# Kernel tuning notes

Hardware: AMD Instinct MI355X
Metric: run time of the kernel (lower is better)

Reference implementation:

```python
import jax, jax.numpy as jnp
import numpy as np

B, T, D, H, Dh, ROT = 2, 2048, 2048, 16, 128, 64
DFF = 4 * D
EPS = 1e-5
NEG = -1e9


def setup_inputs() -> dict:
    key = jax.random.key(0)
    ks = jax.random.split(key, 8)
    s = lambda k, shape, sc: jax.random.normal(k, shape, jnp.float32) * sc
    return {
        "x": s(ks[0], (B, T, D), 1.0),
        "ln_scale": jnp.ones((D,), jnp.float32),
        "ln_offset": jnp.zeros((D,), jnp.float32),
        "wq": s(ks[1], (D, D), 0.02),
        "wk": s(ks[2], (D, D), 0.02),
        "wv": s(ks[3], (D, D), 0.02),
        "wo": s(ks[4], (D, D), 0.02),
        "w1": s(ks[5], (D, DFF), 0.02),
        "b1": jnp.zeros((DFF,), jnp.float32),
        "w2": s(ks[6], (DFF, D), 0.02),
        "b2": jnp.zeros((D,), jnp.float32),
    }


def reference(x, ln_scale, ln_offset, wq, wk, wv, wo, w1, b1, w2, b2):
    def ln(h):  # ReplicatedLayerNorm, fp32 internal; note: same params used twice (shared self.norm)
        h32 = h.astype(jnp.float32)
        m = jnp.mean(h32, axis=-1, keepdims=True)
        v = jnp.var(h32, axis=-1, keepdims=True)
        y = (h32 - m) * jax.lax.rsqrt(v + EPS)
        return (y * ln_scale + ln_offset).astype(h.dtype)

    xn = ln(x)
    q = (xn @ wq).reshape(B, T, H, Dh)
    k = (xn @ wk).reshape(B, T, H, Dh)
    v = (xn @ wv).reshape(B, T, H, Dh)

    # GPT-J interleaved RoPE on first ROT dims
    pos = jnp.arange(T, dtype=jnp.float32)
    inv_freq = 1.0 / (10000.0 ** (jnp.arange(0, ROT, 2, dtype=jnp.float32) / ROT))
    freqs = pos[:, None] * inv_freq[None, :]            # (T, ROT/2)
    cos = jnp.repeat(jnp.cos(freqs), 2, axis=-1)[None, :, None, :]  # (1,T,1,ROT)
    sin = jnp.repeat(jnp.sin(freqs), 2, axis=-1)[None, :, None, :]

    def rope(t):
        tr, tp = t[..., :ROT], t[..., ROT:]
        x1 = tr[..., 0::2]
        x2 = tr[..., 1::2]
        rot_half = jnp.stack((-x2, x1), axis=-1).reshape(tr.shape)
        return jnp.concatenate([tr * cos + rot_half * sin, tp], axis=-1)

    q, k = rope(q), rope(k)

    scale = 1.0 / jnp.sqrt(jnp.float32(Dh))
    scores = jnp.einsum('bthd,bshd->bhts', q, k) * scale
    mask = jnp.where(jnp.tril(jnp.ones((T, T), bool)), 0.0, NEG).astype(scores.dtype)
    w = jax.nn.softmax(scores + mask, axis=-1)
    ctx = jnp.einsum('bhts,bshd->bthd', w, v).reshape(B, T, D)
    x1_ = x + ctx @ wo

    xn2 = ln(x1_)
    h = jax.nn.gelu(xn2.astype(jnp.float32) @ w1 + b1)  # default approximate gelu, as in source
    ff = (h @ w2 + b2).astype(x.dtype)
    return x1_ + ff
```

## Files before the change

kernel.cpp:

```cpp
#include <hip/hip_runtime.h>
#include <hip/hip_bf16.h>

#define B_   2
#define T_   2048
#define D_   2048
#define H_   16
#define DH_  128
#define DFF_ 8192

typedef __attribute__((ext_vector_type(8))) short bf16x8;
typedef __attribute__((ext_vector_type(4))) float f32x4;

__device__ __forceinline__ short f2bf(float f) {
    __hip_bfloat16 h = __float2bfloat16(f);
    return *reinterpret_cast<short*>(&h);
}

__device__ __forceinline__ void gload_lds16(const void* g, void* l) {
    __builtin_amdgcn_global_load_lds(
        (const __attribute__((address_space(1))) void*)g,
        (__attribute__((address_space(3))) void*)l,
        16, 0, 0);
}

__device__ __forceinline__ float gelu_tanh(float x) {
    float x3 = x * x * x;
    return 0.5f * x * (1.f + tanhf(0.7978845608028654f * (x + 0.044715f * x3)));
}

#define MFMA32(a, b, c) __builtin_amdgcn_mfma_f32_16x16x32_bf16((a), (b), (c), 0, 0, 0)

__global__ __launch_bounds__(256) void transpose_cvt(const float* __restrict__ in,
                                                     __hip_bfloat16* __restrict__ out,
                                                     int K, int N, int out_ld, int out_row0)
{
    __shared__ float t[32][65];
    const int n0 = blockIdx.x * 64, k0 = blockIdx.y * 32;
    const int tid = threadIdx.x;
    {
        int kr = tid >> 4;
        int nc = (tid & 15) * 4;
        const float* src = in + (size_t)(k0 + kr) * N + n0 + nc;
        float4 a = *reinterpret_cast<const float4*>(src);
        float4 b = *reinterpret_cast<const float4*>(src + (size_t)16 * N);
        t[kr][nc] = a.x; t[kr][nc + 1] = a.y; t[kr][nc + 2] = a.z; t[kr][nc + 3] = a.w;
        t[kr + 16][nc] = b.x; t[kr + 16][nc + 1] = b.y; t[kr + 16][nc + 2] = b.z; t[kr + 16][nc + 3] = b.w;
    }
    __syncthreads();
    {
        int n  = tid >> 2;
        int kc = (tid & 3) * 8;
        __hip_bfloat16 ob[8];
#pragma unroll
        for (int j = 0; j < 8; ++j) ob[j] = __float2bfloat16(t[kc + j][n]);
        *reinterpret_cast<uint4*>(out + (size_t)(out_row0 + n0 + n) * out_ld + k0 + kc) =
            *reinterpret_cast<uint4*>(ob);
    }
}

__global__ __launch_bounds__(256) void ln_kernel(const float* __restrict__ x,
                                                 const float* __restrict__ sc,
                                                 const float* __restrict__ of,
                                                 __hip_bfloat16* __restrict__ out)
{
    int row = blockIdx.x, tid = threadIdx.x;
    const float* xr = x + (size_t)row * D_;
    float4 v0 = reinterpret_cast<const float4*>(xr)[tid * 2];
    float4 v1 = reinterpret_cast<const float4*>(xr)[tid * 2 + 1];
    float vv[8] = {v0.x, v0.y, v0.z, v0.w, v1.x, v1.y, v1.z, v1.w};
    float s = 0.f, ss = 0.f;
#pragma unroll
    for (int j = 0; j < 8; ++j) { s += vv[j]; ss += vv[j] * vv[j]; }
    for (int o = 32; o; o >>= 1) { s += __shfl_down(s, o); ss += __shfl_down(ss, o); }
    __shared__ float red[8];
    int wid = tid >> 6, lane = tid & 63;
    if (!lane) { red[wid] = s; red[4 + wid] = ss; }
    __syncthreads();
    s  = red[0] + red[1] + red[2] + red[3];
    ss = red[4] + red[5] + red[6] + red[7];
    float mean = s * (1.f / D_);
    float var  = ss * (1.f / D_) - mean * mean;
    float rstd = rsqrtf(var + 1e-5f);
    int c0 = tid * 8;
    __hip_bfloat16 ob[8];
#pragma unroll
    for (int j = 0; j < 8; ++j)
        ob[j] = __float2bfloat16((vv[j] - mean) * rstd * sc[c0 + j] + of[c0 + j]);
    *reinterpret_cast<uint4*>(out + (size_t)row * D_ + c0) = *reinterpret_cast<uint4*>(ob);
}

template<int EPI, int BM>
__global__ __launch_bounds__(512, 2) void gemm8p(
    const __hip_bfloat16* __restrict__ A, const __hip_bfloat16* __restrict__ BT,
    void* __restrict__ Cout, const float* __restrict__ bias,
    const float* __restrict__ resid, int M, int N, int K)
{
    constexpr int MFR = BM / 32;
    constexpr int AUL = BM / 128;
    constexpr int VMC = AUL + 2;
    __shared__ short As[2 * 2 * BM * 32];
    __shared__ short Bs[2 * 2 * 256 * 32];

    const int tid = threadIdx.x;
    const int wid = tid >> 6, lane = tid & 63;
    const int lo = lane & 15, hi = lane >> 4;
    const int wr = wid >> 2, wc = wid & 3;

    const int gx = gridDim.x;
    const int nwg = gx * gridDim.y;
    const int bid = blockIdx.y * gx + blockIdx.x;
    const int swz = (bid & 7) * (nwg >> 3) + (bid >> 3);
    const int m0 = (swz / gx) * BM, n0 = (swz % gx) * 256;

    auto stageA = [&](int tt, int ks) {
#pragma unroll
        for (int l = 0; l < AUL; ++l) {
            int c    = l * 512 + tid;
            int row  = c >> 2, ksub = c & 3;
            int kc   = tt * 64 + ks * 32 + ((ksub ^ ((row >> 1) & 3)) << 3);
            int c0   = l * 512 + wid * 64;
            gload_lds16(A + (size_t)(m0 + row) * K + kc,
                        (char*)As + ((tt & 1) * 2 + ks) * (BM * 64) + c0 * 16);
        }
    };
    auto stageB = [&](int tt, int ks) {
#pragma unroll
        for (int l = 0; l < 2; ++l) {
            int c    = l * 512 + tid;
            int row  = c >> 2, ksub = c & 3;
            int kc   = tt * 64 + ks * 32 + ((ksub ^ ((row >> 1) & 3)) << 3);
            int c0   = l * 512 + wid * 64;
            gload_lds16(BT + (size_t)(n0 + row) * K + kc,
                        (char*)Bs + ((tt & 1) * 2 + ks) * 16384 + c0 * 16);
        }
    };

    const int fsw  = (hi ^ ((lo >> 1) & 3)) << 4;
    const int arow = wr * (BM / 2) + lo;
    const int brow = wc * 64 + lo;

    f32x4 acc[MFR][4] = {};
    const int NT = K >> 6;

    stageA(0, 0); stageB(0, 0); stageA(0, 1); stageB(0, 1);
    asm volatile("s_waitcnt vmcnt(%0)" :: "i"(VMC) : "memory");
    __builtin_amdgcn_s_barrier();
    __builtin_amdgcn_sched_barrier(0);

#define PHASE_MFMA(J)                                                         \
        __builtin_amdgcn_s_barrier();                                         \
        asm volatile("s_waitcnt lgkmcnt(0)" ::: "memory");                    \
        __builtin_amdgcn_sched_barrier(0);                                    \
        __builtin_amdgcn_s_setprio(1);                                        \
        _Pragma("unroll")                                                     \
        for (int m = 0; m < MFR; ++m) {                                       \
            acc[m][J]     = MFMA32(af[m], b0, acc[m][J]);                     \
            acc[m][J + 1] = MFMA32(af[m], b1, acc[m][J + 1]);                 \
        }                                                                     \
        __builtin_amdgcn_s_setprio(0);

#pragma unroll 2
    for (int t = 0; t < NT; ++t) {
        const int bsel = t & 1;
        const bool pf = (t + 1 < NT);
        const char* Ab = (const char*)As + bsel * (2 * BM * 64);
        const char* Bb = (const char*)Bs + bsel * 32768;
        bf16x8 af[MFR], b0, b1;

#pragma unroll
        for (int m = 0; m < MFR; ++m)
            af[m] = *reinterpret_cast<const bf16x8*>(Ab + (arow + m * 16) * 64 + fsw);
        b0 = *reinterpret_cast<const bf16x8*>(Bb + brow * 64 + fsw);
        b1 = *reinterpret_cast<const bf16x8*>(Bb + (brow + 16) * 64 + fsw);
        if (pf) stageA(t + 1, 0);
        PHASE_MFMA(0)
        __builtin_amdgcn_s_barrier();
        __builtin_amdgcn_sched_barrier(0);

        b0 = *reinterpret_cast<const bf16x8*>(Bb + (brow + 32) * 64 + fsw);
        b1 = *reinterpret_cast<const bf16x8*>(Bb + (brow + 48) * 64 + fsw);
        if (pf) stageB(t + 1, 0);
        PHASE_MFMA(2)
        asm volatile("s_waitcnt vmcnt(%0)" :: "i"(VMC) : "memory");
        __builtin_amdgcn_s_barrier();
        __builtin_amdgcn_sched_barrier(0);

#pragma unroll
        for (int m = 0; m < MFR; ++m)
            af[m] = *reinterpret_cast<const bf16x8*>(Ab + BM * 64 + (arow + m * 16) * 64 + fsw);
        b0 = *reinterpret_cast<const bf16x8*>(Bb + 16384 + brow * 64 + fsw);
        b1 = *reinterpret_cast<const bf16x8*>(Bb + 16384 + (brow + 16) * 64 + fsw);
        if (pf) stageA(t + 1, 1);
        PHASE_MFMA(0)
        __builtin_amdgcn_s_barrier();
        __builtin_amdgcn_sched_barrier(0);

        b0 = *reinterpret_cast<const bf16x8*>(Bb + 16384 + (brow + 32) * 64 + fsw);
        b1 = *reinterpret_cast<const bf16x8*>(Bb + 16384 + (brow + 48) * 64 + fsw);
        if (pf) stageB(t + 1, 1);
        PHASE_MFMA(2)
        asm volatile("s_waitcnt vmcnt(%0)" :: "i"(VMC) : "memory");
        __builtin_amdgcn_s_barrier();
        __builtin_amdgcn_sched_barrier(0);
    }
#undef PHASE_MFMA

    float* Cf = (float*)Cout;
    __hip_bfloat16* Cb = (__hip_bfloat16*)Cout;
#pragma unroll
    for (int m = 0; m < MFR; ++m) {
        int rbase = m0 + wr * (BM / 2) + m * 16 + hi * 4;
#pragma unroll
        for (int j = 0; j < 4; ++j) {
            int col = n0 + wc * 64 + (j >> 1) * 32 + (j & 1) * 16 + lo;
            float bv = (EPI == 2 || EPI == 3) ? bias[col] : 0.f;
#pragma unroll
            for (int i = 0; i < 4; ++i) {
                size_t idx = (size_t)(rbase + i) * N + col;
                float v = acc[m][j][i];
                if (EPI == 2 || EPI == 3) v += bv;
                if (EPI == 2) v = gelu_tanh(v);
                if (EPI == 1 || EPI == 3) v += resid[idx];
                if (EPI == 0 || EPI == 2) Cb[idx] = __float2bfloat16(v);
                else                      Cf[idx] = v;
            }
        }
    }
}

__global__ __launch_bounds__(256) void rope_kernel(__hip_bfloat16* __restrict__ qkv)
{
    int idx = blockIdx.x * 256 + threadIdx.x;
    int p  = idx & 31;
    int h  = (idx >> 5) & (H_ - 1);
    int bt = idx >> 9;
    int t  = bt & (T_ - 1);
    float invf = exp2f((float)p * -0.4152410118609203f);
    float fr = (float)t * invf;
    float cs, sn;
    __sincosf(fr, &sn, &cs);
    size_t base = (size_t)bt * (3 * D_) + h * DH_ + 2 * p;
#pragma unroll
    for (int qk = 0; qk < 2; ++qk) {
        uint* pp = reinterpret_cast<uint*>(qkv + base + qk * D_);
        uint u = *pp;
        float x1 = __uint_as_float(u << 16);
        float x2 = __uint_as_float(u & 0xffff0000u);
        short r0 = f2bf(x1 * cs - x2 * sn);
        short r1 = f2bf(x2 * cs + x1 * sn);
        *pp = ((uint)(unsigned short)r0) | (((uint)(unsigned short)r1) << 16);
    }
}

__global__ __launch_bounds__(512) void attn_kernel(const __hip_bfloat16* __restrict__ qkv,
                                                   __hip_bfloat16* __restrict__ ctx)
{
    constexpr int LDQ = 3 * D_;
    constexpr int SV  = 68;

    int idx = blockIdx.y * 16 + blockIdx.x;
    int swz = (idx & 7) * 64 + (idx >> 3);
    const int bh  = swz >> 4;
    const int bxr = 15 - (swz & 15);
    const int b = bh >> 4, h = bh & 15;
    const int tq0 = bxr * 128;

    const int tid = threadIdx.x, wid = tid >> 6, lane = tid & 63;
    const int lo = lane & 15, hi = lane >> 4;
    const int t0 = tq0 + wid * 16;

    __shared__ short Ks[2][64 * 128];
    __shared__ short VsT[128 * SV];

    const __hip_bfloat16* qrow = qkv + (size_t)(b * T_ + t0 + lo) * LDQ + h * DH_;
    bf16x8 qf[4];
#pragma unroll
    for (int dk = 0; dk < 4; ++dk)
        qf[dk] = *reinterpret_cast<const bf16x8*>(qrow + dk * 32 + hi * 8);

    f32x4 octx[8] = {};
    float mreg = -1e30f, lreg = 0.f;

    const size_t kvrow0 = (size_t)(b * T_) * LDQ + h * DH_;
    const int nst = 2 * (bxr + 1);

    bf16x8 vr[2];

#define STAGE_K(s0v, buf)                                                     \
    do {                                                                      \
        _Pragma("unroll")                                                     \
        for (int i = 0; i < 2; ++i) {                                         \
            int c    = i * 512 + tid;                                         \
            int sr   = c >> 4;                                                \
            int cbs  = ((c & 15) * 16) ^ ((sr & 7) << 4);                     \
            gload_lds16(qkv + kvrow0 + (size_t)((s0v) + sr) * LDQ + D_ + (cbs >> 1), \
                        &Ks[buf][c * 8]);                                     \
        }                                                                     \
    } while (0)

#define LOAD_V(s0v)                                                           \
    do {                                                                      \
        _Pragma("unroll")                                                     \
        for (int it = 0; it < 2; ++it) {                                      \
            int c = it * 512 + tid;                                           \
            int s = c >> 4, dc = c & 15;                                      \
            vr[it] = *reinterpret_cast<const bf16x8*>(                        \
                qkv + kvrow0 + (size_t)((s0v) + s) * LDQ + 2 * D_ + dc * 8);  \
        }                                                                     \
    } while (0)

    STAGE_K(0, 0);
    LOAD_V(0);

    for (int st = 0; st < nst; ++st) {
        const int s0 = st * 64;
        const int cur = st & 1;
        __syncthreads();

#pragma unroll
        for (int it = 0; it < 2; ++it) {
            int c = it * 512 + tid;
            int s = c >> 4, dc = c & 15;
            int sswz = s ^ ((dc & 15) << 2);
            short* dst = &VsT[(dc * 8) * SV + sswz];
#pragma unroll
            for (int j = 0; j < 8; ++j)
                dst[j * SV] = vr[it][j];
        }
        if (st + 1 < nst) {
            STAGE_K(s0 + 64, cur ^ 1);
            LOAD_V(s0 + 64);
        }
        asm volatile("s_waitcnt lgkmcnt(0)" ::: "memory");
        __builtin_amdgcn_s_barrier();
        __builtin_amdgcn_sched_barrier(0);

        f32x4 sfr[4] = {};
        __builtin_amdgcn_s_setprio(1);
#pragma unroll
        for (int f = 0; f < 4; ++f) {
            int srow = f * 16 + lo;
            int sw = (srow & 7) << 4;
#pragma unroll
            for (int dk = 0; dk < 4; ++dk) {
                bf16x8 kf = *reinterpret_cast<const bf16x8*>(
                    (const char*)&Ks[cur][0] + srow * 256 + ((dk * 64 + hi * 16) ^ sw));
                sfr[f] = MFMA32(kf, qf[dk], sfr[f]);
            }
        }
        __builtin_amdgcn_s_setprio(0);

        const float qsc = 0.08838834764831845f;
#pragma unroll
        for (int f = 0; f < 4; ++f)
#pragma unroll
            for (int i = 0; i < 4; ++i)
                sfr[f][i] *= qsc;
        if (st >= nst - 2) {
#pragma unroll
            for (int f = 0; f < 4; ++f)
#pragma unroll
                for (int i = 0; i < 4; ++i)
                    if (s0 + f * 16 + hi * 4 + i > t0 + lo) sfr[f][i] = -1e30f;
        }

        float mx = -1e30f;
#pragma unroll
        for (int f = 0; f < 4; ++f)
#pragma unroll
            for (int i = 0; i < 4; ++i)
                mx = fmaxf(mx, sfr[f][i]);
        mx = fmaxf(mx, __shfl_xor(mx, 16));
        mx = fmaxf(mx, __shfl_xor(mx, 32));
        float mn = fmaxf(mreg, mx);
        float ps = __expf(mreg - mn);
        mreg = mn;
        float sum = 0.f;
#pragma unroll
        for (int f = 0; f < 4; ++f)
#pragma unroll
            for (int i = 0; i < 4; ++i) {
                sfr[f][i] = __expf(sfr[f][i] - mn);
                sum += sfr[f][i];
            }
        sum += __shfl_xor(sum, 16);
        sum += __shfl_xor(sum, 32);
        lreg = lreg * ps + sum;

        float psq[4];
#pragma unroll
        for (int i = 0; i < 4; ++i)
            psq[i] = __shfl(ps, hi * 4 + i);
#pragma unroll
        for (int f8 = 0; f8 < 8; ++f8)
#pragma unroll
            for (int i = 0; i < 4; ++i)
                octx[f8][i] *= psq[i];

#pragma unroll
        for (int ks = 0; ks < 2; ++ks) {
            union { bf16x8 v; short s[8]; } pa;
#pragma unroll
            for (int j = 0; j < 4; ++j) {
                pa.s[j]     = f2bf(sfr[2 * ks][j]);
                pa.s[j + 4] = f2bf(sfr[2 * ks + 1][j]);
            }
            __builtin_amdgcn_s_setprio(1);
#pragma unroll
            for (int f8 = 0; f8 < 8; ++f8) {
                int d = f8 * 16 + lo;
                int sw2 = ((d >> 3) & 15) << 2;
                const short* vrow = &VsT[d * SV];
                union { bf16x8 v; uint2 u[2]; } vb;
                vb.u[0] = *reinterpret_cast<const uint2*>(vrow + ((ks * 32 + hi * 4) ^ sw2));
                vb.u[1] = *reinterpret_cast<const uint2*>(vrow + ((ks * 32 + 16 + hi * 4) ^ sw2));
                octx[f8] = MFMA32(pa.v, vb.v, octx[f8]);
            }
            __builtin_amdgcn_s_setprio(0);
        }
    }
#undef STAGE_K
#undef LOAD_V

    float linv[4];
#pragma unroll
    for (int i = 0; i < 4; ++i)
        linv[i] = 1.f / __shfl(lreg, hi * 4 + i);
#pragma unroll
    for (int i = 0; i < 4; ++i) {
        size_t rb = (size_t)(b * T_ + t0 + hi * 4 + i) * D_ + h * DH_;
#pragma unroll
        for (int f8 = 0; f8 < 8; ++f8)
            ctx[rb + f8 * 16 + lo] = __float2bfloat16(octx[f8][i] * linv[i]);
    }
}

extern "C" void kernel_launch(void* const* d_in, const int* in_sizes, int n_in,
                              void* d_out, int out_size, void* d_ws, size_t ws_size,
                              hipStream_t stream)
{
    (void)in_sizes; (void)n_in; (void)out_size; (void)ws_size;
    const float* x   = (const float*)d_in[0];
    const float* lns = (const float*)d_in[1];
    const float* lno = (const float*)d_in[2];
    const float* wq  = (const float*)d_in[3];
    const float* wk  = (const float*)d_in[4];
    const float* wv  = (const float*)d_in[5];
    const float* wo  = (const float*)d_in[6];
    const float* w1  = (const float*)d_in[7];
    const float* b1  = (const float*)d_in[8];
    const float* w2  = (const float*)d_in[9];
    const float* b2  = (const float*)d_in[10];
    float* out = (float*)d_out;

    char* ws = (char*)d_ws;
    __hip_bfloat16* wqkvT = (__hip_bfloat16*)(ws);
    __hip_bfloat16* woT   = (__hip_bfloat16*)(ws + 25165824);
    __hip_bfloat16* w1T   = (__hip_bfloat16*)(ws + 33554432);
    __hip_bfloat16* w2T   = (__hip_bfloat16*)(ws + 67108864);
    __hip_bfloat16* xn    = (__hip_bfloat16*)(ws + 100663296);
    __hip_bfloat16* qkv   = (__hip_bfloat16*)(ws + 117440512);
    __hip_bfloat16* hbuf  = qkv;
    __hip_bfloat16* ctx   = (__hip_bfloat16*)(ws + 167772160);
    float*          x1    = (float*)(ws + 184549376);

    transpose_cvt<<<dim3(32, 64),  256, 0, stream>>>(wq, wqkvT, 2048, 2048, 2048, 0);
    transpose_cvt<<<dim3(32, 64),  256, 0, stream>>>(wk, wqkvT, 2048, 2048, 2048, 2048);
    transpose_cvt<<<dim3(32, 64),  256, 0, stream>>>(wv, wqkvT, 2048, 2048, 2048, 4096);
    transpose_cvt<<<dim3(32, 64),  256, 0, stream>>>(wo, woT,   2048, 2048, 2048, 0);
    transpose_cvt<<<dim3(128, 64), 256, 0, stream>>>(w1, w1T,   2048, 8192, 2048, 0);
    transpose_cvt<<<dim3(32, 256), 256, 0, stream>>>(w2, w2T,   8192, 2048, 8192, 0);

    ln_kernel<<<4096, 256, 0, stream>>>(x, lns, lno, xn);
    gemm8p<0, 128><<<dim3(24, 32), 512, 0, stream>>>(xn, wqkvT, qkv, nullptr, nullptr, 4096, 6144, 2048);
    rope_kernel<<<8192, 256, 0, stream>>>(qkv);
    attn_kernel<<<dim3(16, 32), 512, 0, stream>>>(qkv, ctx);
    gemm8p<1, 128><<<dim3(8, 32), 512, 0, stream>>>(ctx, woT, x1, nullptr, x, 4096, 2048, 2048);
    ln_kernel<<<4096, 256, 0, stream>>>(x1, lns, lno, xn);
    gemm8p<2, 256><<<dim3(32, 16), 512, 0, stream>>>(xn, w1T, hbuf, b1, nullptr, 4096, 8192, 2048);
    gemm8p<3, 128><<<dim3(8, 32), 512, 0, stream>>>(hbuf, w2T, out, b2, x1, 4096, 2048, 8192);
}
```

Baseline: 769.6 us.

## Replace GEMM with 128x128 tile kernel, fuse RoPE into QKV epilogue, lazy softmax rescale

Replaces the 256-wide, multi-phase GEMM with a simpler 128x128-tile kernel. It has one stage per k-slice, launch bounds raised to 4 blocks per CU, and twice as many workgroups per GEMM. RoPE moves out of its own kernel into the QKV GEMM epilogue, using lane shuffles to pair interleaved columns, which saves a full read and write of q and k. The attention kernel skips the running-max rescale of the output accumulator unless the max has grown by more than 8. Smaller tiles cut per-block reuse and raise global traffic, and the lazy rescale allows somewhat larger exponent values before normalisation.

```diff
diff --git a/kernel.cpp b/kernel.cpp
--- a/kernel.cpp
+++ b/kernel.cpp
@@ -89,17 +89,14 @@
     *reinterpret_cast<uint4*>(out + (size_t)row * D_ + c0) = *reinterpret_cast<uint4*>(ob);
 }
 
-template<int EPI, int BM>
-__global__ __launch_bounds__(512, 2) void gemm8p(
+template<int EPI>
+__global__ __launch_bounds__(512, 4) void gemmq(
     const __hip_bfloat16* __restrict__ A, const __hip_bfloat16* __restrict__ BT,
     void* __restrict__ Cout, const float* __restrict__ bias,
     const float* __restrict__ resid, int M, int N, int K)
 {
-    constexpr int MFR = BM / 32;
-    constexpr int AUL = BM / 128;
-    constexpr int VMC = AUL + 2;
-    __shared__ short As[2 * 2 * BM * 32];
-    __shared__ short Bs[2 * 2 * 256 * 32];
+    __shared__ short As[2 * 2 * 128 * 32];
+    __shared__ short Bs[2 * 2 * 128 * 32];
 
     const int tid = threadIdx.x;
     const int wid = tid >> 6, lane = tid & 63;
@@ -110,114 +107,104 @@
     const int nwg = gx * gridDim.y;
     const int bid = blockIdx.y * gx + blockIdx.x;
     const int swz = (bid & 7) * (nwg >> 3) + (bid >> 3);
-    const int m0 = (swz / gx) * BM, n0 = (swz % gx) * 256;
-
+    const int m0 = (swz / gx) * 128, n0 = (swz % gx) * 128;
+
+    const int srow = tid >> 2, sslot = tid & 3;
     auto stageA = [&](int tt, int ks) {
-#pragma unroll
-        for (int l = 0; l < AUL; ++l) {
-            int c    = l * 512 + tid;
-            int row  = c >> 2, ksub = c & 3;
-            int kc   = tt * 64 + ks * 32 + ((ksub ^ ((row >> 1) & 3)) << 3);
-            int c0   = l * 512 + wid * 64;
-            gload_lds16(A + (size_t)(m0 + row) * K + kc,
-                        (char*)As + ((tt & 1) * 2 + ks) * (BM * 64) + c0 * 16);
-        }
+        int kc = tt * 64 + ks * 32 + ((sslot ^ ((srow >> 1) & 3)) << 3);
+        gload_lds16(A + (size_t)(m0 + srow) * K + kc,
+                    (char*)As + ((tt & 1) * 2 + ks) * 8192 + wid * 1024);
     };
     auto stageB = [&](int tt, int ks) {
-#pragma unroll
-        for (int l = 0; l < 2; ++l) {
-            int c    = l * 512 + tid;
-            int row  = c >> 2, ksub = c & 3;
-            int kc   = tt * 64 + ks * 32 + ((ksub ^ ((row >> 1) & 3)) << 3);
-            int c0   = l * 512 + wid * 64;
-            gload_lds16(BT + (size_t)(n0 + row) * K + kc,
-                        (char*)Bs + ((tt & 1) * 2 + ks) * 16384 + c0 * 16);
-        }
+        int kc = tt * 64 + ks * 32 + ((sslot ^ ((srow >> 1) & 3)) << 3);
+        gload_lds16(BT + (size_t)(n0 + srow) * K + kc,
+                    (char*)Bs + ((tt & 1) * 2 + ks) * 8192 + wid * 1024);
     };
 
     const int fsw  = (hi ^ ((lo >> 1) & 3)) << 4;
-    const int arow = wr * (BM / 2) + lo;
-    const int brow = wc * 64 + lo;
-
-    f32x4 acc[MFR][4] = {};
+    const int arow = wr * 64 + lo;
+    const int brow = wc * 32 + lo;
+
+    f32x4 acc[4][2] = {};
     const int NT = K >> 6;
 
     stageA(0, 0); stageB(0, 0); stageA(0, 1); stageB(0, 1);
-    asm volatile("s_waitcnt vmcnt(%0)" :: "i"(VMC) : "memory");
+    asm volatile("s_waitcnt vmcnt(2)" ::: "memory");
     __builtin_amdgcn_s_barrier();
     __builtin_amdgcn_sched_barrier(0);
-
-#define PHASE_MFMA(J)                                                         \
-        __builtin_amdgcn_s_barrier();                                         \
-        asm volatile("s_waitcnt lgkmcnt(0)" ::: "memory");                    \
-        __builtin_amdgcn_sched_barrier(0);                                    \
-        __builtin_amdgcn_s_setprio(1);                                        \
-        _Pragma("unroll")                                                     \
-        for (int m = 0; m < MFR; ++m) {                                       \
-            acc[m][J]     = MFMA32(af[m], b0, acc[m][J]);                     \
-            acc[m][J + 1] = MFMA32(af[m], b1, acc[m][J + 1]);                 \
-        }                                                                     \
-        __builtin_amdgcn_s_setprio(0);
 
 #pragma unroll 2
     for (int t = 0; t < NT; ++t) {
         const int bsel = t & 1;
         const bool pf = (t + 1 < NT);
-        const char* Ab = (const char*)As + bsel * (2 * BM * 64);
-        const char* Bb = (const char*)Bs + bsel * 32768;
-        bf16x8 af[MFR], b0, b1;
-
-#pragma unroll
-        for (int m = 0; m < MFR; ++m)
-            af[m] = *reinterpret_cast<const bf16x8*>(Ab + (arow + m * 16) * 64 + fsw);
-        b0 = *reinterpret_cast<const bf16x8*>(Bb + brow * 64 + fsw);
-        b1 = *reinterpret_cast<const bf16x8*>(Bb + (brow + 16) * 64 + fsw);
-        if (pf) stageA(t + 1, 0);
-        PHASE_MFMA(0)
-        __builtin_amdgcn_s_barrier();
-        __builtin_amdgcn_sched_barrier(0);
-
-        b0 = *reinterpret_cast<const bf16x8*>(Bb + (brow + 32) * 64 + fsw);
-        b1 = *reinterpret_cast<const bf16x8*>(Bb + (brow + 48) * 64 + fsw);
-        if (pf) stageB(t + 1, 0);
-        PHASE_MFMA(2)
-        asm volatile("s_waitcnt vmcnt(%0)" :: "i"(VMC) : "memory");
-        __builtin_amdgcn_s_barrier();
-        __builtin_amdgcn_sched_barrier(0);
-
-#pragma unroll
-        for (int m = 0; m < MFR; ++m)
-            af[m] = *reinterpret_cast<const bf16x8*>(Ab + BM * 64 + (arow + m * 16) * 64 + fsw);
-        b0 = *reinterpret_cast<const bf16x8*>(Bb + 16384 + brow * 64 + fsw);
-        b1 = *reinterpret_cast<const bf16x8*>(Bb + 16384 + (brow + 16) * 64 + fsw);
-        if (pf) stageA(t + 1, 1);
-        PHASE_MFMA(0)
-        __builtin_amdgcn_s_barrier();
-        __builtin_amdgcn_sched_barrier(0);
-
-        b0 = *reinterpret_cast<const bf16x8*>(Bb + 16384 + (brow + 32) * 64 + fsw);
-        b1 = *reinterpret_cast<const bf16x8*>(Bb + 16384 + (brow + 48) * 64 + fsw);
-        if (pf) stageB(t + 1, 1);
-        PHASE_MFMA(2)
-        asm volatile("s_waitcnt vmcnt(%0)" :: "i"(VMC) : "memory");
-        __builtin_amdgcn_s_barrier();
-        __builtin_amdgcn_sched_barrier(0);
-    }
-#undef PHASE_MFMA
+        const char* Ab = (const char*)As + bsel * 16384;
+        const char* Bb = (const char*)Bs + bsel * 16384;
+
+#pragma unroll
+        for (int ks = 0; ks < 2; ++ks) {
+            bf16x8 af[4], b0, b1;
+#pragma unroll
+            for (int m = 0; m < 4; ++m)
+                af[m] = *reinterpret_cast<const bf16x8*>(
+                    Ab + ks * 8192 + (arow + m * 16) * 64 + fsw);
+            b0 = *reinterpret_cast<const bf16x8*>(Bb + ks * 8192 + brow * 64 + fsw);
+            b1 = *reinterpret_cast<const bf16x8*>(Bb + ks * 8192 + (brow + 16) * 64 + fsw);
+            if (pf) { stageA(t + 1, ks); stageB(t + 1, ks); }
+            asm volatile("s_waitcnt lgkmcnt(0)" ::: "memory");
+            __builtin_amdgcn_sched_barrier(0);
+            __builtin_amdgcn_s_setprio(1);
+#pragma unroll
+            for (int m = 0; m < 4; ++m) {
+                acc[m][0] = MFMA32(af[m], b0, acc[m][0]);
+                acc[m][1] = MFMA32(af[m], b1, acc[m][1]);
+            }
+            __builtin_amdgcn_s_setprio(0);
+            if (pf) asm volatile("s_waitcnt vmcnt(2)" ::: "memory");
+            else    asm volatile("s_waitcnt vmcnt(0)" ::: "memory");
+            __builtin_amdgcn_s_barrier();
+            __builtin_amdgcn_sched_barrier(0);
+        }
+    }
 
     float* Cf = (float*)Cout;
     __hip_bfloat16* Cb = (__hip_bfloat16*)Cout;
-#pragma unroll
-    for (int m = 0; m < MFR; ++m) {
-        int rbase = m0 + wr * (BM / 2) + m * 16 + hi * 4;
-#pragma unroll
-        for (int j = 0; j < 4; ++j) {
-            int col = n0 + wc * 64 + (j >> 1) * 32 + (j & 1) * 16 + lo;
+
+    bool doRope = false;
+    float invf[2];
+    if (EPI == 4) {
+        doRope = (n0 < 4096) && (wc < 2);
+        if (doRope) {
+#pragma unroll
+            for (int j = 0; j < 2; ++j) {
+                int p = (wc * 32 + j * 16 + lo) >> 1;
+                invf[j] = exp2f((float)p * -0.4152410118609203f);
+            }
+        }
+    }
+
+#pragma unroll
+    for (int m = 0; m < 4; ++m) {
+        int rbase = m0 + wr * 64 + m * 16 + hi * 4;
+#pragma unroll
+        for (int j = 0; j < 2; ++j) {
+            int col = n0 + wc * 32 + j * 16 + lo;
             float bv = (EPI == 2 || EPI == 3) ? bias[col] : 0.f;
 #pragma unroll
             for (int i = 0; i < 4; ++i) {
                 size_t idx = (size_t)(rbase + i) * N + col;
                 float v = acc[m][j][i];
+                if (EPI == 4) {
+                    if (doRope) {
+                        float pv = __shfl_xor(v, 1);
+                        int tt = (rbase + i) & (T_ - 1);
+                        float fr = (float)tt * invf[j];
+                        float cs, sn;
+                        __sincosf(fr, &sn, &cs);
+                        v = (lo & 1) ? (v * cs + pv * sn) : (v * cs - pv * sn);
+                    }
+                    Cb[idx] = __float2bfloat16(v);
+                    continue;
+                }
                 if (EPI == 2 || EPI == 3) v += bv;
                 if (EPI == 2) v = gelu_tanh(v);
                 if (EPI == 1 || EPI == 3) v += resid[idx];
@@ -225,30 +212,6 @@
                 else                      Cf[idx] = v;
             }
         }
-    }
-}
-
-__global__ __launch_bounds__(256) void rope_kernel(__hip_bfloat16* __restrict__ qkv)
-{
-    int idx = blockIdx.x * 256 + threadIdx.x;
-    int p  = idx & 31;
-    int h  = (idx >> 5) & (H_ - 1);
-    int bt = idx >> 9;
-    int t  = bt & (T_ - 1);
-    float invf = exp2f((float)p * -0.4152410118609203f);
-    float fr = (float)t * invf;
-    float cs, sn;
-    __sincosf(fr, &sn, &cs);
-    size_t base = (size_t)bt * (3 * D_) + h * DH_ + 2 * p;
-#pragma unroll
-    for (int qk = 0; qk < 2; ++qk) {
-        uint* pp = reinterpret_cast<uint*>(qkv + base + qk * D_);
-        uint u = *pp;
-        float x1 = __uint_as_float(u << 16);
-        float x2 = __uint_as_float(u & 0xffff0000u);
-        short r0 = f2bf(x1 * cs - x2 * sn);
-        short r1 = f2bf(x2 * cs + x1 * sn);
-        *pp = ((uint)(unsigned short)r0) | (((uint)(unsigned short)r1) << 16);
     }
 }
 
@@ -372,30 +335,34 @@
                 mx = fmaxf(mx, sfr[f][i]);
         mx = fmaxf(mx, __shfl_xor(mx, 16));
         mx = fmaxf(mx, __shfl_xor(mx, 32));
-        float mn = fmaxf(mreg, mx);
-        float ps = __expf(mreg - mn);
-        mreg = mn;
+
+        if (!__all(mx - mreg <= 8.f)) {
+            float mn = fmaxf(mreg, mx);
+            float ps = __expf(mreg - mn);
+            mreg = mn;
+            lreg *= ps;
+            float psq[4];
+#pragma unroll
+            for (int i = 0; i < 4; ++i)
+                psq[i] = __shfl(ps, hi * 4 + i);
+#pragma unroll
+            for (int f8 = 0; f8 < 8; ++f8)
+#pragma unroll
+                for (int i = 0; i < 4; ++i)
+                    octx[f8][i] *= psq[i];
+        }
+
         float sum = 0.f;
 #pragma unroll
         for (int f = 0; f < 4; ++f)
 #pragma unroll
             for (int i = 0; i < 4; ++i) {
-                sfr[f][i] = __expf(sfr[f][i] - mn);
+                sfr[f][i] = __expf(sfr[f][i] - mreg);
                 sum += sfr[f][i];
             }
         sum += __shfl_xor(sum, 16);
         sum += __shfl_xor(sum, 32);
-        lreg = lreg * ps + sum;
-
-        float psq[4];
-#pragma unroll
-        for (int i = 0; i < 4; ++i)
-            psq[i] = __shfl(ps, hi * 4 + i);
-#pragma unroll
-        for (int f8 = 0; f8 < 8; ++f8)
-#pragma unroll
-            for (int i = 0; i < 4; ++i)
-                octx[f8][i] *= psq[i];
+        lreg += sum;
 
 #pragma unroll
         for (int ks = 0; ks < 2; ++ks) {
@@ -472,11 +439,10 @@
     transpose_cvt<<<dim3(32, 256), 256, 0, stream>>>(w2, w2T,   8192, 2048, 8192, 0);
 
     ln_kernel<<<4096, 256, 0, stream>>>(x, lns, lno, xn);
-    gemm8p<0, 128><<<dim3(24, 32), 512, 0, stream>>>(xn, wqkvT, qkv, nullptr, nullptr, 4096, 6144, 2048);
-    rope_kernel<<<8192, 256, 0, stream>>>(qkv);
+    gemmq<4><<<dim3(48, 32), 512, 0, stream>>>(xn, wqkvT, qkv, nullptr, nullptr, 4096, 6144, 2048);
     attn_kernel<<<dim3(16, 32), 512, 0, stream>>>(qkv, ctx);
-    gemm8p<1, 128><<<dim3(8, 32), 512, 0, stream>>>(ctx, woT, x1, nullptr, x, 4096, 2048, 2048);
+    gemmq<1><<<dim3(16, 32), 512, 0, stream>>>(ctx, woT, x1, nullptr, x, 4096, 2048, 2048);
     ln_kernel<<<4096, 256, 0, stream>>>(x1, lns, lno, xn);
-    gemm8p<2, 256><<<dim3(32, 16), 512, 0, stream>>>(xn, w1T, hbuf, b1, nullptr, 4096, 8192, 2048);
-    gemm8p<3, 128><<<dim3(8, 32), 512, 0, stream>>>(hbuf, w2T, out, b2, x1, 4096, 2048, 8192);
-}
+    gemmq<2><<<dim3(64, 32), 512, 0, stream>>>(xn, w1T, hbuf, b1, nullptr, 4096, 8192, 2048);
+    gemmq<3><<<dim3(16, 32), 512, 0, stream>>>(hbuf, w2T, out, b2, x1, 4096, 2048, 8192);
+}
```

After: 757.1 us. No clear change (-1.6%).
